# Kernel tuning notes

Measured on AMD Instinct MI355X. Metric: run time of the kernel, lower is better.

The kernel has to match this reference:

```python
import jax, jax.numpy as jnp
import numpy as np

HIDDEN = 1024

def setup_inputs() -> dict:
    key = jax.random.key(0)
    k1, k2, k3 = jax.random.split(key, 3)
    H = HIDDEN
    # xavier_uniform for [H, 4H] kernels: bound = sqrt(6/(H+4H))
    bound = float(np.sqrt(6.0 / (H + 4 * H)))
    x = jax.random.normal(k1, (32, 512, H), dtype=jnp.float32)
    input_kernel = jax.random.uniform(k2, (H, 4 * H), dtype=jnp.float32, minval=-bound, maxval=bound)
    hidden_kernel = jax.random.uniform(k3, (H, 4 * H), dtype=jnp.float32, minval=-bound, maxval=bound)
    bias = jnp.zeros((4 * H,), dtype=jnp.float32)
    return {"x": x, "input_kernel": input_kernel, "hidden_kernel": hidden_kernel, "bias": bias}

def _lstm(x, input_kernel, hidden_kernel, bias):
    B, S, H = x.shape
    # Precompute input projection for all timesteps as one big GEMM: [B,S,4H]
    xg = jnp.einsum('bsh,hg->bsg', x, input_kernel) + bias
    h0 = jnp.zeros((B, H), dtype=x.dtype)
    c0 = jnp.zeros((B, H), dtype=x.dtype)

    def step(carry, xg_t):
        h, c = carry
        gates = xg_t + h @ hidden_kernel  # [B, 4H]
        i_g, f_g, g_g, o_g = jnp.split(gates, 4, axis=-1)
        c = jax.nn.sigmoid(f_g) * c + jax.nn.sigmoid(i_g) * jnp.tanh(g_g)
        h = jax.nn.sigmoid(o_g) * jnp.tanh(c)
        return (h, c), h

    # scan over time axis: move S to leading dim
    (_, _), hs = jax.lax.scan(step, (h0, c0), jnp.swapaxes(xg, 0, 1))
    return jnp.swapaxes(hs, 0, 1)  # [B, S, H]

def reference(x, input_kernel, hidden_kernel, bias):
    return _lstm(x, input_kernel, hidden_kernel, bias)
```

## Files before the change

kernel.cpp:

```cpp
#include <hip/hip_runtime.h>


typedef __attribute__((ext_vector_type(4))) float f32x4_t;
typedef __attribute__((ext_vector_type(8))) short bf16x8_t;
typedef unsigned long long ull_t;

#define HID   1024
#define SLEN  512
#define NGATE 4096

#define XG_OFF    0ULL
#define RING_OFF  134217728ULL
#define WIT_OFF   167772160ULL
#define WHT_OFF   176160768ULL
#define FLAGS_OFF 184680448ULL
#define XB_OFF    RING_OFF

#define NBLK_B      256
#define SLOT_SHORTS 32768

__device__ __forceinline__ unsigned short f2bf(float f) {
  unsigned u = __float_as_uint(f);
  u += 0x7fffu + ((u >> 16) & 1u);
  return (unsigned short)(u >> 16);
}
__device__ __forceinline__ float bf2f(unsigned short u) {
  return __uint_as_float(((unsigned)u) << 16);
}
__device__ __forceinline__ float fast_rcp(float x) { return __builtin_amdgcn_rcpf(x); }
__device__ __forceinline__ float sigmoid_f(float x) { return fast_rcp(1.f + __expf(-x)); }
__device__ __forceinline__ float tanh_f(float x) { return 1.f - 2.f * fast_rcp(1.f + __expf(2.f * x)); }

__global__ __launch_bounds__(256) void conv_x_bf16(const float* __restrict__ in,
                                                   unsigned short* __restrict__ out) {
  size_t i = (size_t)blockIdx.x * 256 + threadIdx.x;
  const float4* p = (const float4*)in;
  float4 v = p[i];
  ushort4 o;
  o.x = f2bf(v.x); o.y = f2bf(v.y); o.z = f2bf(v.z); o.w = f2bf(v.w);
  ((ushort4*)out)[i] = o;
}

__global__ void transpose_w_bf16(const float* __restrict__ in,
                                 unsigned short* __restrict__ out) {
  __shared__ float tile[32][33];
  int tx = threadIdx.x, ty = threadIdx.y;
  int n0 = blockIdx.x * 32, k0 = blockIdx.y * 32;
  #pragma unroll
  for (int i = 0; i < 4; i++)
    tile[ty + 8 * i][tx] = in[(size_t)(k0 + ty + 8 * i) * NGATE + n0 + tx];
  __syncthreads();
  #pragma unroll
  for (int i = 0; i < 4; i++)
    out[(size_t)(n0 + ty + 8 * i) * HID + k0 + tx] = f2bf(tile[tx][ty + 8 * i]);
}

__global__ void init_ws(unsigned* __restrict__ flags) {
  int i = threadIdx.x;
  flags[i] = 0u;
}

__global__ __launch_bounds__(256) void gemm_xg(const unsigned short* __restrict__ A,
                                               const unsigned short* __restrict__ BT,
                                               unsigned short* __restrict__ C) {
  extern __shared__ char smem[];
  char* As = smem;
  char* Bs = smem + 10240;
  const int tid = threadIdx.x;
  const int lane = tid & 63, w = tid >> 6, q = lane >> 4, l16 = lane & 15;
  const int wm = w & 1, wn = w >> 1;
  const size_t m0 = (size_t)blockIdx.y * 128, n0 = (size_t)blockIdx.x * 128;

  f32x4_t acc[4][4];
  #pragma unroll
  for (int i = 0; i < 4; i++)
    #pragma unroll
    for (int j = 0; j < 4; j++) acc[i][j] = (f32x4_t){0.f, 0.f, 0.f, 0.f};

  for (int kk = 0; kk < 32; kk++) {
    const int k0 = kk * 32;
    #pragma unroll
    for (int h = 0; h < 2; h++) {
      int idx = tid + h * 256;
      int r = idx >> 2, ch = idx & 3;
      uint4 va = *(const uint4*)((const char*)A + ((m0 + r) * HID + k0) * 2 + ch * 16);
      *(uint4*)(As + r * 80 + ch * 16) = va;
      uint4 vb = *(const uint4*)((const char*)BT + ((n0 + r) * HID + k0) * 2 + ch * 16);
      *(uint4*)(Bs + r * 80 + ch * 16) = vb;
    }
    __syncthreads();
    bf16x8_t af[4], bf[4];
    #pragma unroll
    for (int mt = 0; mt < 4; mt++)
      af[mt] = *(const bf16x8_t*)(As + (wm * 64 + mt * 16 + l16) * 80 + q * 16);
    #pragma unroll
    for (int nt = 0; nt < 4; nt++)
      bf[nt] = *(const bf16x8_t*)(Bs + (wn * 64 + nt * 16 + l16) * 80 + q * 16);
    #pragma unroll
    for (int mt = 0; mt < 4; mt++)
      #pragma unroll
      for (int nt = 0; nt < 4; nt++)
        acc[mt][nt] = __builtin_amdgcn_mfma_f32_16x16x32_bf16(af[mt], bf[nt], acc[mt][nt], 0, 0, 0);
    __syncthreads();
  }

  unsigned short* cst = (unsigned short*)smem;
  #pragma unroll
  for (int mt = 0; mt < 4; mt++)
    #pragma unroll
    for (int nt = 0; nt < 4; nt++)
      #pragma unroll
      for (int r = 0; r < 4; r++) {
        int m = wm * 64 + mt * 16 + q * 4 + r;
        int n = wn * 64 + nt * 16 + l16;
        cst[m * 136 + n] = f2bf(acc[mt][nt][r]);
      }
  __syncthreads();
  #pragma unroll
  for (int i = 0; i < 8; i++) {
    int idx = tid + i * 256;
    int row = idx >> 4, ch = idx & 15;
    uint4 v = *(const uint4*)((const char*)cst + row * 272 + ch * 16);
    *(uint4*)((char*)C + ((m0 + row) * NGATE + n0) * 2 + ch * 16) = v;
  }
}

__global__ __launch_bounds__(256, 1) void lstm_persistent(
    const unsigned short* __restrict__ xg,
    const unsigned short* __restrict__ whT,
    const float* __restrict__ bias,
    float* __restrict__ out,
    unsigned short* ring,
    unsigned* flags) {
  __shared__ __align__(16) char h_lds[8 * 2064];
  __shared__ float gates[16 * 65];

  const int tid = threadIdx.x;
  const int lane = tid & 63, wv = tid >> 6, q = lane >> 4, l16 = lane & 15;
  const int g = blockIdx.x >> 6;
  const int m = blockIdx.x & 63;
  const int b_l = tid >> 4, j_l = tid & 15;

  bf16x8_t bfr[32];
  {
    const char* wrow = (const char*)whT +
        ((size_t)(wv * 1024 + m * 16 + l16) * HID) * 2 + q * 16;
    #pragma unroll
    for (int kk = 0; kk < 32; kk++)
      bfr[kk] = *(const bf16x8_t*)(wrow + kk * 64);
    #pragma unroll
    for (int kk = 0; kk < 32; kk++)
      asm volatile("" : "+v"(bfr[kk]));
  }
  float bsr[4];
  #pragma unroll
  for (int G = 0; G < 4; G++) bsr[G] = bias[G * 1024 + m * 16 + j_l];
  float c_st = 0.f;
  const char* arow = h_lds + (l16 & 7) * 2064 + q * 16;
  unsigned short* ring_g = ring + (size_t)g * 8192;
  unsigned* fl_g = flags + g * 64;

  for (int t = 0; t < SLEN; t++) {
    unsigned short xgv[4];
    if (tid < 128) {
      const unsigned short* p =
          xg + ((size_t)(g * 8 + b_l) * 512 + t) * 4096 + m * 16 + j_l;
      xgv[0] = p[0]; xgv[1] = p[1024]; xgv[2] = p[2048]; xgv[3] = p[3072];
    }
    if (t > 0) {
      if (tid < 64) {
        const unsigned* fp = fl_g + tid;
        while (__hip_atomic_load(fp, __ATOMIC_RELAXED, __HIP_MEMORY_SCOPE_AGENT) < (unsigned)t)
          __builtin_amdgcn_s_sleep(1);
      }
      __syncthreads();
      asm volatile("" ::: "memory");
      {
        const char* src = (const char*)(ring_g + (size_t)(t - 1) * SLOT_SHORTS);
        uint4 v0 = *(const uint4*)(src + tid * 16);
        uint4 v1 = *(const uint4*)(src + tid * 16 + 4096);
        uint4 v2 = *(const uint4*)(src + tid * 16 + 8192);
        uint4 v3 = *(const uint4*)(src + tid * 16 + 12288);
        int c0 = tid, c1 = tid + 256, c2 = tid + 512, c3 = tid + 768;
        *(uint4*)(h_lds + (c0 >> 7) * 2064 + (c0 & 127) * 16) = v0;
        *(uint4*)(h_lds + (c1 >> 7) * 2064 + (c1 & 127) * 16) = v1;
        *(uint4*)(h_lds + (c2 >> 7) * 2064 + (c2 & 127) * 16) = v2;
        *(uint4*)(h_lds + (c3 >> 7) * 2064 + (c3 & 127) * 16) = v3;
      }
    }
    __syncthreads();

    f32x4_t acc0 = (f32x4_t){0.f, 0.f, 0.f, 0.f};
    f32x4_t acc1 = (f32x4_t){0.f, 0.f, 0.f, 0.f};
    if (t > 0) {
      #pragma unroll
      for (int kk = 0; kk < 32; kk += 2) {
        bf16x8_t a0 = *(const bf16x8_t*)(arow + kk * 64);
        bf16x8_t a1 = *(const bf16x8_t*)(arow + kk * 64 + 64);
        acc0 = __builtin_amdgcn_mfma_f32_16x16x32_bf16(a0, bfr[kk], acc0, 0, 0, 0);
        acc1 = __builtin_amdgcn_mfma_f32_16x16x32_bf16(a1, bfr[kk + 1], acc1, 0, 0, 0);
      }
    }
    #pragma unroll
    for (int r = 0; r < 4; r++) {
      int bb = q * 4 + r;
      gates[bb * 65 + wv * 16 + l16] = acc0[r] + acc1[r];
    }
    __syncthreads();

    if (tid < 128) {
      float gi = gates[b_l * 65 + j_l]      + bsr[0] + bf2f(xgv[0]);
      float gf = gates[b_l * 65 + 16 + j_l] + bsr[1] + bf2f(xgv[1]);
      float gg = gates[b_l * 65 + 32 + j_l] + bsr[2] + bf2f(xgv[2]);
      float go = gates[b_l * 65 + 48 + j_l] + bsr[3] + bf2f(xgv[3]);
      float i_s = sigmoid_f(gi), f_s = sigmoid_f(gf);
      float g_t = tanh_f(gg), o_s = sigmoid_f(go);
      c_st = f_s * c_st + i_s * g_t;
      float h = o_s * tanh_f(c_st);
      unsigned short hb = f2bf(h);
      unsigned other = __shfl_xor((unsigned)hb, 1);
      unsigned u = ((unsigned)hb & 0xffffu) | (other << 16);
      unsigned u2 = __shfl_xor(u, 2);
      if ((j_l & 3) == 0) {
        ull_t v8 = (ull_t)u | ((ull_t)u2 << 32);
        ull_t* dst = (ull_t*)(ring_g + (size_t)t * SLOT_SHORTS +
                              b_l * 1024 + m * 16 + j_l);
        __hip_atomic_store(dst, v8, __ATOMIC_RELAXED, __HIP_MEMORY_SCOPE_AGENT);
      }
      asm volatile("" ::: "memory");
      out[((size_t)(g * 8 + b_l) * 512 + t) * 1024 + m * 16 + j_l] = h;
    }
    asm volatile("s_waitcnt vmcnt(1)" ::: "memory");
    __syncthreads();
    if (tid == 0)
      __hip_atomic_store(fl_g + m, (unsigned)(t + 1),
                         __ATOMIC_RELAXED, __HIP_MEMORY_SCOPE_AGENT);
  }
}

extern "C" void kernel_launch(void* const* d_in, const int* in_sizes, int n_in,
                              void* d_out, int out_size, void* d_ws, size_t ws_size,
                              hipStream_t stream) {
  const float* x    = (const float*)d_in[0];
  const float* wi   = (const float*)d_in[1];
  const float* wh   = (const float*)d_in[2];
  const float* bias = (const float*)d_in[3];
  float* out = (float*)d_out;

  char* ws = (char*)d_ws;
  unsigned short* xg   = (unsigned short*)(ws + XG_OFF);
  unsigned short* xb   = (unsigned short*)(ws + XB_OFF);
  unsigned short* ring = (unsigned short*)(ws + RING_OFF);
  unsigned short* wiT  = (unsigned short*)(ws + WIT_OFF);
  unsigned short* whT  = (unsigned short*)(ws + WHT_OFF);
  unsigned* flags      = (unsigned*)(ws + FLAGS_OFF);

  conv_x_bf16<<<16384, 256, 0, stream>>>(x, xb);
  transpose_w_bf16<<<dim3(128, 32), dim3(32, 8), 0, stream>>>(wi, wiT);
  transpose_w_bf16<<<dim3(128, 32), dim3(32, 8), 0, stream>>>(wh, whT);
  init_ws<<<1, 256, 0, stream>>>(flags);
  gemm_xg<<<dim3(32, 128), 256, 34816, stream>>>(xb, wiT, xg);
  lstm_persistent<<<NBLK_B, 256, 0, stream>>>(xg, whT, bias, out, ring, flags);
}
```

Baseline: 2.168 ms.

## Halve persistent LSTM blocks, doubling hidden units per block and padding flags

The persistent recurrent kernel now uses 32 blocks per batch group instead of 64, so each block owns 32 hidden units and holds twice as many recurrent weight fragments in registers. This halves the number of producers each block must wait on per timestep and puts all 256 threads to work on the elementwise gate math. Flags are spaced four words apart to reduce false sharing between spinning readers. In exchange, each block does twice the MFMA work per step and register pressure rises sharply (64 bf16x8 fragments), which risks spills.

After: 2.086 ms. -3.7%, faster.

```diff
diff --git a/kernel.cpp b/kernel.cpp
--- a/kernel.cpp
+++ b/kernel.cpp
@@ -16,7 +16,8 @@
 #define FLAGS_OFF 184680448ULL
 #define XB_OFF    RING_OFF
 
-#define NBLK_B      256
+#define NBLK_B      128
+#define FLAG_STRIDE 4
 #define SLOT_SHORTS 32768
 
 __device__ __forceinline__ unsigned short f2bf(float f) {
@@ -58,6 +59,7 @@
 __global__ void init_ws(unsigned* __restrict__ flags) {
   int i = threadIdx.x;
   flags[i] = 0u;
+  flags[i + 256] = 0u;
 }
 
 __global__ __launch_bounds__(256) void gemm_xg(const unsigned short* __restrict__ A,
@@ -133,43 +135,46 @@
     unsigned short* ring,
     unsigned* flags) {
   __shared__ __align__(16) char h_lds[8 * 2064];
-  __shared__ float gates[16 * 65];
+  __shared__ float gates[16 * 132];
 
   const int tid = threadIdx.x;
   const int lane = tid & 63, wv = tid >> 6, q = lane >> 4, l16 = lane & 15;
-  const int g = blockIdx.x >> 6;
-  const int m = blockIdx.x & 63;
-  const int b_l = tid >> 4, j_l = tid & 15;
-
-  bf16x8_t bfr[32];
+  const int g = blockIdx.x >> 5;
+  const int m = blockIdx.x & 31;
+  const int b_l = tid >> 5, j_l = tid & 31;
+
+  bf16x8_t bfr[64];
   {
-    const char* wrow = (const char*)whT +
-        ((size_t)(wv * 1024 + m * 16 + l16) * HID) * 2 + q * 16;
-    #pragma unroll
-    for (int kk = 0; kk < 32; kk++)
-      bfr[kk] = *(const bf16x8_t*)(wrow + kk * 64);
-    #pragma unroll
-    for (int kk = 0; kk < 32; kk++)
-      asm volatile("" : "+v"(bfr[kk]));
+    #pragma unroll
+    for (int nt = 0; nt < 2; nt++) {
+      const char* wrow = (const char*)whT +
+          ((size_t)(wv * 1024 + m * 32 + nt * 16 + l16) * HID) * 2 + q * 16;
+      #pragma unroll
+      for (int kk = 0; kk < 32; kk++)
+        bfr[nt * 32 + kk] = *(const bf16x8_t*)(wrow + kk * 64);
+    }
+    #pragma unroll
+    for (int i = 0; i < 64; i++)
+      asm volatile("" : "+v"(bfr[i]));
   }
   float bsr[4];
   #pragma unroll
-  for (int G = 0; G < 4; G++) bsr[G] = bias[G * 1024 + m * 16 + j_l];
+  for (int G = 0; G < 4; G++) bsr[G] = bias[G * 1024 + m * 32 + j_l];
   float c_st = 0.f;
   const char* arow = h_lds + (l16 & 7) * 2064 + q * 16;
   unsigned short* ring_g = ring + (size_t)g * 8192;
-  unsigned* fl_g = flags + g * 64;
+  unsigned* fl_g = flags + g * 32 * FLAG_STRIDE;
 
   for (int t = 0; t < SLEN; t++) {
     unsigned short xgv[4];
-    if (tid < 128) {
+    {
       const unsigned short* p =
-          xg + ((size_t)(g * 8 + b_l) * 512 + t) * 4096 + m * 16 + j_l;
+          xg + ((size_t)(g * 8 + b_l) * 512 + t) * 4096 + m * 32 + j_l;
       xgv[0] = p[0]; xgv[1] = p[1024]; xgv[2] = p[2048]; xgv[3] = p[3072];
     }
     if (t > 0) {
-      if (tid < 64) {
-        const unsigned* fp = fl_g + tid;
+      if (tid < 32) {
+        const unsigned* fp = fl_g + tid * FLAG_STRIDE;
         while (__hip_atomic_load(fp, __ATOMIC_RELAXED, __HIP_MEMORY_SCOPE_AGENT) < (unsigned)t)
           __builtin_amdgcn_s_sleep(1);
       }
@@ -190,29 +195,34 @@
     }
     __syncthreads();
 
-    f32x4_t acc0 = (f32x4_t){0.f, 0.f, 0.f, 0.f};
-    f32x4_t acc1 = (f32x4_t){0.f, 0.f, 0.f, 0.f};
+    f32x4_t a00 = (f32x4_t){0.f, 0.f, 0.f, 0.f};
+    f32x4_t a01 = (f32x4_t){0.f, 0.f, 0.f, 0.f};
+    f32x4_t a10 = (f32x4_t){0.f, 0.f, 0.f, 0.f};
+    f32x4_t a11 = (f32x4_t){0.f, 0.f, 0.f, 0.f};
     if (t > 0) {
       #pragma unroll
       for (int kk = 0; kk < 32; kk += 2) {
-        bf16x8_t a0 = *(const bf16x8_t*)(arow + kk * 64);
-        bf16x8_t a1 = *(const bf16x8_t*)(arow + kk * 64 + 64);
-        acc0 = __builtin_amdgcn_mfma_f32_16x16x32_bf16(a0, bfr[kk], acc0, 0, 0, 0);
-        acc1 = __builtin_amdgcn_mfma_f32_16x16x32_bf16(a1, bfr[kk + 1], acc1, 0, 0, 0);
+        bf16x8_t x0 = *(const bf16x8_t*)(arow + kk * 64);
+        bf16x8_t x1 = *(const bf16x8_t*)(arow + kk * 64 + 64);
+        a00 = __builtin_amdgcn_mfma_f32_16x16x32_bf16(x0, bfr[kk], a00, 0, 0, 0);
+        a10 = __builtin_amdgcn_mfma_f32_16x16x32_bf16(x0, bfr[32 + kk], a10, 0, 0, 0);
+        a01 = __builtin_amdgcn_mfma_f32_16x16x32_bf16(x1, bfr[kk + 1], a01, 0, 0, 0);
+        a11 = __builtin_amdgcn_mfma_f32_16x16x32_bf16(x1, bfr[32 + kk + 1], a11, 0, 0, 0);
       }
     }
     #pragma unroll
     for (int r = 0; r < 4; r++) {
       int bb = q * 4 + r;
-      gates[bb * 65 + wv * 16 + l16] = acc0[r] + acc1[r];
-    }
-    __syncthreads();
-
-    if (tid < 128) {
-      float gi = gates[b_l * 65 + j_l]      + bsr[0] + bf2f(xgv[0]);
-      float gf = gates[b_l * 65 + 16 + j_l] + bsr[1] + bf2f(xgv[1]);
-      float gg = gates[b_l * 65 + 32 + j_l] + bsr[2] + bf2f(xgv[2]);
-      float go = gates[b_l * 65 + 48 + j_l] + bsr[3] + bf2f(xgv[3]);
+      gates[bb * 132 + wv * 32 + l16]      = a00[r] + a01[r];
+      gates[bb * 132 + wv * 32 + 16 + l16] = a10[r] + a11[r];
+    }
+    __syncthreads();
+
+    {
+      float gi = gates[b_l * 132 + j_l]      + bsr[0] + bf2f(xgv[0]);
+      float gf = gates[b_l * 132 + 32 + j_l] + bsr[1] + bf2f(xgv[1]);
+      float gg = gates[b_l * 132 + 64 + j_l] + bsr[2] + bf2f(xgv[2]);
+      float go = gates[b_l * 132 + 96 + j_l] + bsr[3] + bf2f(xgv[3]);
       float i_s = sigmoid_f(gi), f_s = sigmoid_f(gf);
       float g_t = tanh_f(gg), o_s = sigmoid_f(go);
       c_st = f_s * c_st + i_s * g_t;
@@ -224,16 +234,16 @@
       if ((j_l & 3) == 0) {
         ull_t v8 = (ull_t)u | ((ull_t)u2 << 32);
         ull_t* dst = (ull_t*)(ring_g + (size_t)t * SLOT_SHORTS +
-                              b_l * 1024 + m * 16 + j_l);
+                              b_l * 1024 + m * 32 + j_l);
         __hip_atomic_store(dst, v8, __ATOMIC_RELAXED, __HIP_MEMORY_SCOPE_AGENT);
       }
       asm volatile("" ::: "memory");
-      out[((size_t)(g * 8 + b_l) * 512 + t) * 1024 + m * 16 + j_l] = h;
+      out[((size_t)(g * 8 + b_l) * 512 + t) * 1024 + m * 32 + j_l] = h;
     }
     asm volatile("s_waitcnt vmcnt(1)" ::: "memory");
     __syncthreads();
     if (tid == 0)
-      __hip_atomic_store(fl_g + m, (unsigned)(t + 1),
+      __hip_atomic_store(fl_g + m * FLAG_STRIDE, (unsigned)(t + 1),
                          __ATOMIC_RELAXED, __HIP_MEMORY_SCOPE_AGENT);
   }
 }
```
